# Performance work log

Measured on AMD Instinct MI355X. Metric: run time of the kernel, lower is better.

Reference implementation:

```python
import jax, jax.numpy as jnp
import numpy as np
from jax import lax

INPUT_SIZE = 64
HIDDEN = 64
LAYERS = 8
B, T = 256, 2048


def setup_inputs() -> dict:
    key = jax.random.key(0)
    ks = jax.random.split(key, 10)
    s = 1.0 / np.sqrt(HIDDEN)  # PyTorch RNN init scale U(-1/sqrt(h), 1/sqrt(h))
    u = lambda k, shape: jax.random.uniform(k, shape, jnp.float32, -s, s)
    return {
        "x": jax.random.normal(ks[0], (B, T, INPUT_SIZE), jnp.float32),
        "h_state": jnp.zeros((LAYERS, B, HIDDEN), jnp.float32),
        "W_ih0": u(ks[1], (HIDDEN, INPUT_SIZE)),        # layer-0 input weights
        "W_ih": u(ks[2], (LAYERS - 1, HIDDEN, HIDDEN)), # layers 1..7 input weights
        "W_hh": u(ks[3], (LAYERS, HIDDEN, HIDDEN)),
        "b_ih": u(ks[4], (LAYERS, HIDDEN)),
        "b_hh": u(ks[5], (LAYERS, HIDDEN)),
        "W_out": u(ks[6], (1, HIDDEN)),
        "b_out": u(ks[7], (1,)),
    }


def reference(x, h_state, W_ih0, W_ih, W_hh, b_ih, b_hh, W_out, b_out):
    # Precompute layer-0 input projection for all timesteps (one big GEMM).
    x_proj = jnp.einsum("bti,hi->bth", x, W_ih0) + b_ih[0]  # [B,T,H]
    xt = jnp.transpose(x_proj, (1, 0, 2))  # [T,B,H]

    def step(h, x_t):
        # h: [LAYERS, B, H]; one timestep of the 8-layer tanh RNN stack
        new_h = []
        inp = None
        for l in range(LAYERS):
            if l == 0:
                pre = x_t + h[0] @ W_hh[0].T + b_hh[0]
            else:
                pre = inp @ W_ih[l - 1].T + b_ih[l] + h[l] @ W_hh[l].T + b_hh[l]
            inp = jnp.tanh(pre)
            new_h.append(inp)
        return jnp.stack(new_h), inp  # carry, top-layer output

    h_final, tops = lax.scan(step, h_state, xt)  # tops: [T,B,H]
    # Batched output projection (replaces the per-timestep Python loop)
    y = jnp.transpose(tops @ W_out.T + b_out, (1, 0, 2))  # [B,T,1]
    return (y, h_final)
```

## Files before the change

kernel.cpp:

```cpp
#include <hip/hip_runtime.h>

typedef _Float16 h2 __attribute__((ext_vector_type(2)));
typedef _Float16 h8 __attribute__((ext_vector_type(8)));
typedef __fp16   g2 __attribute__((ext_vector_type(2)));
typedef __fp16   g8 __attribute__((ext_vector_type(8)));
typedef float    f32x4 __attribute__((ext_vector_type(4)));

#define TT 2048
#define HH 64
#define NL 8
#define NB 256
#define G  16
#define NCH (TT/G)
#define NI  (NCH + NL)

#define PRP 20

union GU { g8 v; g2 p[4]; h8 h; };

#define PH_BASE(l, P) (((l)*2 + (P)) * 2048)
#define CH_OFF(j, c)  ((j)*128 + ((((c) ^ ((j)&7))) * 16))

__device__ __forceinline__ float tanh_fast(float v){
    float e = __expf(2.0f * v);
    float r = __builtin_amdgcn_rcpf(e + 1.0f);
    return fmaf(-2.0f, r, 1.0f);
}

__device__ __forceinline__ void barrier_lgkm_only(){
    asm volatile("" ::: "memory");
    __builtin_amdgcn_s_waitcnt(0xc07f);
    __builtin_amdgcn_s_barrier();
    asm volatile("" ::: "memory");
}


#define INTERVAL(MM, P, XC, XN) { \
    const int mm = (MM); \
    const bool act = (unsigned)(mm - wv) < (unsigned)NCH; \
    if (wv == 0){ \
        if (mm + 1 < NCH){ \
            _Pragma("unroll") \
            for (int j = 0; j < G; ++j) \
                *(_Float16*)(BB + PH_BASE(0, 1-(P)) + j*128 + (((lane>>3)^(j&7))*16) + (lane&7)*2) = (_Float16)XC[j]; \
        } \
        if (mm + 2 < NCH){ \
            _Pragma("unroll") \
            for (int j = 0; j < G; ++j) \
                XN[j] = x[((size_t)b*TT + (size_t)(mm+2)*G + j)*HH + lane]; \
        } \
    } \
    if (wv == 7 && mm >= 8){ \
         \
        GU ha0, ha1; \
        ha0.h = *(const h8*)(BB + PH_BASE(8, P) + CH_OFF(nn, g)); \
        ha1.h = *(const h8*)(BB + PH_BASE(8, P) + CH_OFF(nn, 4+g)); \
        f32x4 ay = {0.f, 0.f, 0.f, 0.f}; \
        ay = __builtin_amdgcn_mfma_f32_16x16x32_f16(ha0.v, woutB[0].v, ay, 0, 0, 0); \
        ay = __builtin_amdgcn_mfma_f32_16x16x32_f16(ha1.v, woutB[1].v, ay, 0, 0, 0); \
        if (nn == 0){ \
            f32x4 st; \
            st[0] = ay[0] + bout; st[1] = ay[1] + bout; \
            st[2] = ay[2] + bout; st[3] = ay[3] + bout; \
            *(f32x4*)(yout + (size_t)b*TT + (size_t)(mm-8)*G + g*4) = st; \
        } \
    } \
    if (act){ \
         \
        GU bx0, bx1; \
        bx0.h = *(const h8*)(BB + PH_BASE(wv, P) + CH_OFF(nn, g)); \
        bx1.h = *(const h8*)(BB + PH_BASE(wv, P) + CH_OFF(nn, 4+g)); \
        f32x4 xd0 = {bs[0],bs[0],bs[0],bs[0]}, xd1 = {bs[1],bs[1],bs[1],bs[1]}; \
        f32x4 xd2 = {bs[2],bs[2],bs[2],bs[2]}, xd3 = {bs[3],bs[3],bs[3],bs[3]}; \
        xd0 = __builtin_amdgcn_mfma_f32_16x16x32_f16(bx0.v, wihA[0][0].v, xd0, 0, 0, 0); \
        xd0 = __builtin_amdgcn_mfma_f32_16x16x32_f16(bx1.v, wihA[0][1].v, xd0, 0, 0, 0); \
        xd1 = __builtin_amdgcn_mfma_f32_16x16x32_f16(bx0.v, wihA[1][0].v, xd1, 0, 0, 0); \
        xd1 = __builtin_amdgcn_mfma_f32_16x16x32_f16(bx1.v, wihA[1][1].v, xd1, 0, 0, 0); \
        xd2 = __builtin_amdgcn_mfma_f32_16x16x32_f16(bx0.v, wihA[2][0].v, xd2, 0, 0, 0); \
        xd2 = __builtin_amdgcn_mfma_f32_16x16x32_f16(bx1.v, wihA[2][1].v, xd2, 0, 0, 0); \
        xd3 = __builtin_amdgcn_mfma_f32_16x16x32_f16(bx0.v, wihA[3][0].v, xd3, 0, 0, 0); \
        xd3 = __builtin_amdgcn_mfma_f32_16x16x32_f16(bx1.v, wihA[3][1].v, xd3, 0, 0, 0); \
         \
        *(f32x4*)(preTf + ((size_t)(wv*16+nn)*4 + 0)*PRP + g*4) = xd0; \
        *(f32x4*)(preTf + ((size_t)(wv*16+nn)*4 + 1)*PRP + g*4) = xd1; \
        *(f32x4*)(preTf + ((size_t)(wv*16+nn)*4 + 2)*PRP + g*4) = xd2; \
        *(f32x4*)(preTf + ((size_t)(wv*16+nn)*4 + 3)*PRP + g*4) = xd3; \
         \
        f32x4 prv0, prv1, prv2, prv3; \
        { \
            const float* pb = preTf + ((size_t)(wv*16+nn)*4 + g)*PRP; \
            prv0 = *(const f32x4*)(pb);      prv1 = *(const f32x4*)(pb + 4); \
            prv2 = *(const f32x4*)(pb + 8);  prv3 = *(const f32x4*)(pb + 12); \
        } \
         \
        _Pragma("unroll") \
        for (int j = 0; j < G; ++j){ \
            GU hA0, hA1; \
            if (j == 0){ hA0 = hp0; hA1 = hp1; } \
            else { \
                hA0.h = *(const h8*)(BB + PH_BASE(wv+1, 1-(P)) + CH_OFF(j-1, g)); \
                hA1.h = *(const h8*)(BB + PH_BASE(wv+1, 1-(P)) + CH_OFF(j-1, 4+g)); \
            } \
            const f32x4 zz = {0.f, 0.f, 0.f, 0.f}; \
            f32x4 a00 = __builtin_amdgcn_mfma_f32_16x16x32_f16(hA0.v, whhB[0][0].v, zz, 0, 0, 0); \
            f32x4 a01 = __builtin_amdgcn_mfma_f32_16x16x32_f16(hA1.v, whhB[0][1].v, zz, 0, 0, 0); \
            f32x4 a10 = __builtin_amdgcn_mfma_f32_16x16x32_f16(hA0.v, whhB[1][0].v, zz, 0, 0, 0); \
            f32x4 a11 = __builtin_amdgcn_mfma_f32_16x16x32_f16(hA1.v, whhB[1][1].v, zz, 0, 0, 0); \
            f32x4 a20 = __builtin_amdgcn_mfma_f32_16x16x32_f16(hA0.v, whhB[2][0].v, zz, 0, 0, 0); \
            f32x4 a21 = __builtin_amdgcn_mfma_f32_16x16x32_f16(hA1.v, whhB[2][1].v, zz, 0, 0, 0); \
            f32x4 a30 = __builtin_amdgcn_mfma_f32_16x16x32_f16(hA0.v, whhB[3][0].v, zz, 0, 0, 0); \
            f32x4 a31 = __builtin_amdgcn_mfma_f32_16x16x32_f16(hA1.v, whhB[3][1].v, zz, 0, 0, 0); \
            const float s0 = a00[0] + a01[0], s1 = a10[0] + a11[0]; \
            const float s2 = a20[0] + a21[0], s3 = a30[0] + a31[0]; \
            const float pa = (g & 2) ? ((g & 1) ? s3 : s2) : ((g & 1) ? s1 : s0); \
            const float prj = (j < 4) ? prv0[j&3] : (j < 8) ? prv1[j&3] \
                             : (j < 12) ? prv2[j&3] : prv3[j&3]; \
            const float hn = tanh_fast(pa + prj); \
            *(_Float16*)(BB + PH_BASE(wv+1, 1-(P)) + j*128 + (((lane>>3)^(j&7))*16) + (lane&7)*2) = (_Float16)hn; \
            if (j == G-1){ \
                 \
                hp0.h = *(const h8*)(BB + PH_BASE(wv+1, 1-(P)) + CH_OFF(G-1, g)); \
                hp1.h = *(const h8*)(BB + PH_BASE(wv+1, 1-(P)) + CH_OFF(G-1, 4+g)); \
            } \
            if (mm - wv == NCH-1 && j == G-1) \
                hout[((size_t)wv*NB + b)*HH + lane] = hn; \
        } \
    } \
    barrier_lgkm_only(); \
}

__global__ void __launch_bounds__(512) rnn_kernel(
    const float* __restrict__ x,
    const float* __restrict__ h_state,
    const float* __restrict__ W_ih0,
    const float* __restrict__ W_ih,
    const float* __restrict__ W_hh,
    const float* __restrict__ b_ih,
    const float* __restrict__ b_hh,
    const float* __restrict__ W_out,
    const float* __restrict__ b_out,
    float* __restrict__ out)
{
    __shared__ __attribute__((aligned(16))) _Float16 buf[(NL+1)*2*G*HH];
    __shared__ __attribute__((aligned(16))) float preT[NL*16*4*PRP];
    char* BB = (char*)buf;
    float* preTf = preT;
    const int tid  = threadIdx.x;
    const int wv   = tid >> 6;
    const int lane = tid & 63;
    const int g    = lane >> 4;
    const int nn   = lane & 15;
    const size_t b = blockIdx.x;

    GU wihA[4][2], whhB[4][2];
    const float* Wi = (wv == 0) ? W_ih0 : (W_ih + (size_t)(wv-1)*HH*HH);
    const float* Wh = W_hh + (size_t)wv*HH*HH;
    #pragma unroll
    for (int t = 0; t < 4; ++t){
        #pragma unroll
        for (int kt = 0; kt < 2; ++kt){
            const float* pi = Wi + (size_t)(t*16 + nn)*HH + kt*32 + g*8;
            const float* ph = Wh + (size_t)(t*16 + nn)*HH + kt*32 + g*8;
            f32x4 i0 = *(const f32x4*)(pi), i1 = *(const f32x4*)(pi + 4);
            f32x4 h0 = *(const f32x4*)(ph), h1 = *(const f32x4*)(ph + 4);
            wihA[t][kt].p[0] = __builtin_amdgcn_cvt_pkrtz(i0[0], i0[1]);
            wihA[t][kt].p[1] = __builtin_amdgcn_cvt_pkrtz(i0[2], i0[3]);
            wihA[t][kt].p[2] = __builtin_amdgcn_cvt_pkrtz(i1[0], i1[1]);
            wihA[t][kt].p[3] = __builtin_amdgcn_cvt_pkrtz(i1[2], i1[3]);
            whhB[t][kt].p[0] = __builtin_amdgcn_cvt_pkrtz(h0[0], h0[1]);
            whhB[t][kt].p[1] = __builtin_amdgcn_cvt_pkrtz(h0[2], h0[3]);
            whhB[t][kt].p[2] = __builtin_amdgcn_cvt_pkrtz(h1[0], h1[1]);
            whhB[t][kt].p[3] = __builtin_amdgcn_cvt_pkrtz(h1[2], h1[3]);
        }
    }
    float bs[4];
    #pragma unroll
    for (int t = 0; t < 4; ++t)
        bs[t] = b_ih[wv*HH + t*16 + nn] + b_hh[wv*HH + t*16 + nn];
    float bout = b_out[0];

    GU woutB[2];
    if (wv == 7){
        #pragma unroll
        for (int kt = 0; kt < 2; ++kt)
            #pragma unroll
            for (int q = 0; q < 4; ++q)
                woutB[kt].p[q] = __builtin_amdgcn_cvt_pkrtz(
                    W_out[kt*32 + g*8 + q*2], W_out[kt*32 + g*8 + q*2 + 1]);
    }

    for (int i = tid; i < (NL+1)*2*G*HH; i += 512) buf[i] = (_Float16)0.f;
    __syncthreads();
    *(_Float16*)(BB + PH_BASE(wv+1, 1-(wv&1)) + (G-1)*128 + (((lane>>3)^((G-1)&7))*16) + (lane&7)*2)
        = (_Float16)h_state[((size_t)wv*NB + b)*HH + lane];
    float xa[G], xb[G];
    if (wv == 0){
        #pragma unroll
        for (int j = 0; j < G; ++j){
            *(_Float16*)(BB + PH_BASE(0, 1) + j*128 + (((lane>>3)^(j&7))*16) + (lane&7)*2)
                = (_Float16)x[((size_t)b*TT + j)*HH + lane];
            xa[j] = x[((size_t)b*TT + G + j)*HH + lane];
        }
    }
    __syncthreads();

    GU hp0, hp1;
    hp0.h = *(const h8*)(BB + PH_BASE(wv+1, 1-(wv&1)) + CH_OFF(G-1, g));
    hp1.h = *(const h8*)(BB + PH_BASE(wv+1, 1-(wv&1)) + CH_OFF(G-1, 4+g));

    float* yout = out;
    float* hout = out + (size_t)NB*TT;

    for (int m2 = 0; m2 < NI; m2 += 2){
        INTERVAL(m2,     1, xa, xb)
        INTERVAL(m2 + 1, 0, xb, xa)
    }
}

extern "C" void kernel_launch(void* const* d_in, const int* in_sizes, int n_in,
                              void* d_out, int out_size, void* d_ws, size_t ws_size,
                              hipStream_t stream) {
    (void)in_sizes; (void)n_in; (void)d_ws; (void)ws_size; (void)out_size;
    const float* x       = (const float*)d_in[0];
    const float* h_state = (const float*)d_in[1];
    const float* W_ih0   = (const float*)d_in[2];
    const float* W_ih    = (const float*)d_in[3];
    const float* W_hh    = (const float*)d_in[4];
    const float* b_ih    = (const float*)d_in[5];
    const float* b_hh    = (const float*)d_in[6];
    const float* W_out   = (const float*)d_in[7];
    const float* b_out   = (const float*)d_in[8];
    float* out = (float*)d_out;

    rnn_kernel<<<dim3(NB), dim3(512), 0, stream>>>(
        x, h_state, W_ih0, W_ih, W_hh, b_ih, b_hh, W_out, b_out, out);
}
```

Before: 487.6 us.

## Replace per-interval block barrier with point-to-point LDS flags between layer waves

```diff
diff --git a/kernel.cpp b/kernel.cpp
--- a/kernel.cpp
+++ b/kernel.cpp
@@ -15,6 +15,7 @@
 #define NI  (NCH + NL)
 
 #define PRP 20
+#define NNS 84
 
 union GU { g8 v; g2 p[4]; h8 h; };
 
@@ -25,13 +26,6 @@
     float e = __expf(2.0f * v);
     float r = __builtin_amdgcn_rcpf(e + 1.0f);
     return fmaf(-2.0f, r, 1.0f);
-}
-
-__device__ __forceinline__ void barrier_lgkm_only(){
-    asm volatile("" ::: "memory");
-    __builtin_amdgcn_s_waitcnt(0xc07f);
-    __builtin_amdgcn_s_barrier();
-    asm volatile("" ::: "memory");
 }
 
 
@@ -66,6 +60,10 @@
         } \
     } \
     if (act){ \
+        if (wv > 0){ \
+            while (((volatile int*)prodF)[wv] < mm) __builtin_amdgcn_s_sleep(1); \
+            asm volatile("" ::: "memory"); \
+        } \
          \
         GU bx0, bx1; \
         bx0.h = *(const h8*)(BB + PH_BASE(wv, P) + CH_OFF(nn, g)); \
@@ -81,16 +79,23 @@
         xd3 = __builtin_amdgcn_mfma_f32_16x16x32_f16(bx0.v, wihA[3][0].v, xd3, 0, 0, 0); \
         xd3 = __builtin_amdgcn_mfma_f32_16x16x32_f16(bx1.v, wihA[3][1].v, xd3, 0, 0, 0); \
          \
-        *(f32x4*)(preTf + ((size_t)(wv*16+nn)*4 + 0)*PRP + g*4) = xd0; \
-        *(f32x4*)(preTf + ((size_t)(wv*16+nn)*4 + 1)*PRP + g*4) = xd1; \
-        *(f32x4*)(preTf + ((size_t)(wv*16+nn)*4 + 2)*PRP + g*4) = xd2; \
-        *(f32x4*)(preTf + ((size_t)(wv*16+nn)*4 + 3)*PRP + g*4) = xd3; \
-         \
+        asm volatile("" ::: "memory"); \
+        ((volatile int*)consF)[wv] = mm; \
+         \
+        *(f32x4*)(preTf + (size_t)(wv*16+nn)*NNS + 0*PRP + g*4) = xd0; \
+        *(f32x4*)(preTf + (size_t)(wv*16+nn)*NNS + 1*PRP + g*4) = xd1; \
+        *(f32x4*)(preTf + (size_t)(wv*16+nn)*NNS + 2*PRP + g*4) = xd2; \
+        *(f32x4*)(preTf + (size_t)(wv*16+nn)*NNS + 3*PRP + g*4) = xd3; \
         f32x4 prv0, prv1, prv2, prv3; \
         { \
-            const float* pb = preTf + ((size_t)(wv*16+nn)*4 + g)*PRP; \
+            const float* pb = preTf + (size_t)(wv*16+nn)*NNS + g*PRP; \
             prv0 = *(const f32x4*)(pb);      prv1 = *(const f32x4*)(pb + 4); \
             prv2 = *(const f32x4*)(pb + 8);  prv3 = *(const f32x4*)(pb + 12); \
+        } \
+         \
+        if (wv < 7){ \
+            while (((volatile int*)consF)[wv+1] < mm-1) __builtin_amdgcn_s_sleep(1); \
+            asm volatile("" ::: "memory"); \
         } \
          \
         _Pragma("unroll") \
@@ -118,15 +123,16 @@
             const float hn = tanh_fast(pa + prj); \
             *(_Float16*)(BB + PH_BASE(wv+1, 1-(P)) + j*128 + (((lane>>3)^(j&7))*16) + (lane&7)*2) = (_Float16)hn; \
             if (j == G-1){ \
-                 \
                 hp0.h = *(const h8*)(BB + PH_BASE(wv+1, 1-(P)) + CH_OFF(G-1, g)); \
                 hp1.h = *(const h8*)(BB + PH_BASE(wv+1, 1-(P)) + CH_OFF(G-1, 4+g)); \
             } \
             if (mm - wv == NCH-1 && j == G-1) \
                 hout[((size_t)wv*NB + b)*HH + lane] = hn; \
         } \
+         \
+        asm volatile("" ::: "memory"); \
+        ((volatile int*)prodF)[wv+1] = mm + 1; \
     } \
-    barrier_lgkm_only(); \
 }
 
 __global__ void __launch_bounds__(512) rnn_kernel(
@@ -142,7 +148,9 @@
     float* __restrict__ out)
 {
     __shared__ __attribute__((aligned(16))) _Float16 buf[(NL+1)*2*G*HH];
-    __shared__ __attribute__((aligned(16))) float preT[NL*16*4*PRP];
+    __shared__ __attribute__((aligned(16))) float preT[NL*16*NNS];
+    __shared__ int prodF[16];
+    __shared__ int consF[16];
     char* BB = (char*)buf;
     float* preTf = preT;
     const int tid  = threadIdx.x;
@@ -190,6 +198,10 @@
     }
 
     for (int i = tid; i < (NL+1)*2*G*HH; i += 512) buf[i] = (_Float16)0.f;
+    if (tid < 16){
+        prodF[tid] = 0;
+        consF[tid] = tid - 2;
+    }
     __syncthreads();
     *(_Float16*)(BB + PH_BASE(wv+1, 1-(wv&1)) + (G-1)*128 + (((lane>>3)^((G-1)&7))*16) + (lane&7)*2)
         = (_Float16)h_state[((size_t)wv*NB + b)*HH + lane];
```

Result: no change. 479.9 us (-1.6%).
